# Performance work log

Measured on AMD Instinct MI355X. Metric: run time of the kernel, lower is better.

## Reference

```python
import jax, jax.numpy as jnp
import numpy as np

N = 50000     # nodes
E = 800000    # edges
D = 64        # hidesize (= out_channels per head)
H = 5         # heads
C = 64        # per-head channels (concat=False -> mean over heads, C == D)
NEG_SLOPE = 0.2
LN_EPS = 1e-5


def setup_inputs() -> dict:
    key = jax.random.key(0)
    ks = jax.random.split(key, 16)
    s = 0.05
    return {
        "features": jax.random.normal(ks[0], (N, D), dtype=jnp.float32),
        "edge_index": jax.random.randint(ks[1], (2, E), 0, N, dtype=jnp.int64),
        "rel_emb_vector": jax.random.normal(ks[2], (E, D), dtype=jnp.float32),
        # GATv2Conv params
        "Wl": jax.random.normal(ks[3], (D, H * C), dtype=jnp.float32) * s,
        "bl": jnp.zeros((H * C,), jnp.float32),
        "Wr": jax.random.normal(ks[4], (D, H * C), dtype=jnp.float32) * s,
        "br": jnp.zeros((H * C,), jnp.float32),
        "We": jax.random.normal(ks[5], (D, H * C), dtype=jnp.float32) * s,  # lin_edge, no bias
        "att": jax.random.normal(ks[6], (H, C), dtype=jnp.float32) * s,
        "conv_bias": jnp.zeros((C,), jnp.float32),
        # LayerNorms
        "ln_g": jnp.ones((D,), jnp.float32), "ln_b": jnp.zeros((D,), jnp.float32),
        "ln1_g": jnp.ones((D,), jnp.float32), "ln1_b": jnp.zeros((D,), jnp.float32),
        # MLP (activation resolved to None by the source bug)
        "fc_w": jax.random.normal(ks[7], (D, 2 * D), dtype=jnp.float32) * s,
        "fc_b": jnp.zeros((2 * D,), jnp.float32),
        "fc1_w": jax.random.normal(ks[8], (2 * D, D), dtype=jnp.float32) * s,
        "fc1_b": jnp.zeros((D,), jnp.float32),
    }


def _layernorm(x, g, b):
    m = x.mean(-1, keepdims=True)
    v = ((x - m) ** 2).mean(-1, keepdims=True)
    return (x - m) * jax.lax.rsqrt(v + LN_EPS) * g + b


def _gatv2_conv(x, edge_index, edge_attr, Wl, bl, Wr, br, We, att, conv_bias):
    src, dst = edge_index[0], edge_index[1]
    n = x.shape[0]
    # add_self_loops with fill_value='mean': self-loop edge_attr = mean of incoming edge_attr
    cnt = jax.ops.segment_sum(jnp.ones((edge_attr.shape[0],), x.dtype), dst, num_segments=n)
    loop_attr = jax.ops.segment_sum(edge_attr, dst, num_segments=n) / jnp.maximum(cnt, 1.0)[:, None]
    ar = jnp.arange(n, dtype=src.dtype)
    src2 = jnp.concatenate([src, ar])
    dst2 = jnp.concatenate([dst, ar])
    ea = jnp.concatenate([edge_attr, loop_attr], axis=0)        # [E+N, D]
    xl = (x @ Wl + bl).reshape(n, H, C)                          # source transform
    xr = (x @ Wr + br).reshape(n, H, C)                          # target transform
    em = (ea @ We).reshape(-1, H, C)
    m = jax.nn.leaky_relu(xl[src2] + xr[dst2] + em, NEG_SLOPE)   # [E+N, H, C]
    logits = jnp.einsum('ehc,hc->eh', m, att)                    # [E+N, H]
    # scatter-softmax over destination nodes (self loops guarantee nonempty segments)
    mx = jax.lax.stop_gradient(jax.ops.segment_max(logits, dst2, num_segments=n))
    z = jnp.exp(logits - mx[dst2])
    den = jax.ops.segment_sum(z, dst2, num_segments=n)
    alpha = z / den[dst2]                                        # [E+N, H]
    out = jax.ops.segment_sum(xl[src2] * alpha[:, :, None], dst2, num_segments=n)  # [N, H, C]
    return out.mean(axis=1) + conv_bias                          # concat=False -> head mean


def reference(features, edge_index, rel_emb_vector, Wl, bl, Wr, br, We, att, conv_bias,
              ln_g, ln_b, ln1_g, ln1_b, fc_w, fc_b, fc1_w, fc1_b):
    conv = _gatv2_conv(features, edge_index, rel_emb_vector, Wl, bl, Wr, br, We, att, conv_bias)
    x = _layernorm(features + conv, ln_g, ln_b)
    h = (x @ fc_w + fc_b) @ fc1_w + fc1_b   # activation=None, dropout in eval mode
    return _layernorm(x + h, ln1_g, ln1_b)
```

## Files before the change

### kernel.cpp

```cpp
#include <hip/hip_runtime.h>
#include <hip/hip_bf16.h>
#include <math.h>

#define LN_EPS 1e-5f
#define NEGS 0.2f

typedef short s8v __attribute__((ext_vector_type(8)));
typedef short s4v __attribute__((ext_vector_type(4)));
typedef float f4v __attribute__((ext_vector_type(4)));
typedef unsigned short ushort;

__device__ __forceinline__ float wredsum(float v) {
#pragma unroll
    for (int s = 32; s > 0; s >>= 1) v += __shfl_xor(v, s);
    return v;
}
__device__ __forceinline__ ushort f2bf(float x) {
    unsigned int u = __float_as_uint(x);
    u += 0x7fffu + ((u >> 16) & 1u);
    return (ushort)(u >> 16);
}
__device__ __forceinline__ float bf2f(ushort u) {
    return __uint_as_float(((unsigned int)u) << 16);
}

__global__ __launch_bounds__(256) void k_prep(const float* __restrict__ Weg,
                                              const float* __restrict__ Wlg,
                                              const float* __restrict__ Wrg,
                                              ushort* __restrict__ weTg,
                                              ushort* __restrict__ wlrTg) {
    int i = blockIdx.x * 256 + threadIdx.x;
    if (i >= 7680) return;
    int mat = i / 2560;
    int j = i - mat * 2560;
    int n = j >> 3, kb = j & 7;
    const float* W = (mat == 0) ? Weg : (mat == 1) ? Wlg : Wrg;
    s8v v;
#pragma unroll
    for (int k = 0; k < 8; k++) v[k] = (short)f2bf(W[(kb * 8 + k) * 320 + n]);
    int by = (n * 128 + kb * 16) ^ ((n & 7) << 4);
    ushort* dstp = (mat == 0) ? weTg : (wlrTg + (mat - 1) * 20480);
    *(s8v*)((char*)dstp + by) = v;
}

__global__ void k_hist(const int* __restrict__ dst, int* __restrict__ cnt, int E) {
    int idx = blockIdx.x * blockDim.x + threadIdx.x;
    int stride = gridDim.x * blockDim.x;
    for (; idx < E; idx += stride) atomicAdd(&cnt[dst[idx]], 1);
}

__global__ __launch_bounds__(1024) void k_scanA(const int* __restrict__ cnt,
                                                int* __restrict__ bsum, int N) {
    __shared__ int ws[16];
    int tt = threadIdx.x, ln = tt & 63, wv = tt >> 6;
    int i = blockIdx.x * 1024 + tt;
    int v = (i < N) ? (cnt[i] + 1) : 0;
#pragma unroll
    for (int s = 32; s > 0; s >>= 1) v += __shfl_xor(v, s);
    if (ln == 0) ws[wv] = v;
    __syncthreads();
    if (tt == 0) {
        int s = 0;
#pragma unroll
        for (int k = 0; k < 16; k++) s += ws[k];
        bsum[blockIdx.x] = s;
    }
}
__global__ __launch_bounds__(64) void k_scanB(const int* __restrict__ bsum,
                                              int* __restrict__ bpre,
                                              int* __restrict__ roffN, int nb) {
    int ln = threadIdx.x;
    int v = (ln < nb) ? bsum[ln] : 0;
    int x = v;
#pragma unroll
    for (int off = 1; off < 64; off <<= 1) {
        int y = __shfl_up(x, off);
        if (ln >= off) x += y;
    }
    if (ln < nb) bpre[ln] = x - v;
    if (ln == 63) *roffN = x;
}
__global__ __launch_bounds__(1024) void k_scanC(const int* __restrict__ cnt,
                                                const int* __restrict__ bpre,
                                                int* __restrict__ roff,
                                                int* __restrict__ wpos, int N) {
    __shared__ int ws[16];
    int tt = threadIdx.x, ln = tt & 63, wv = tt >> 6;
    int i = blockIdx.x * 1024 + tt;
    int v = (i < N) ? (cnt[i] + 1) : 0;
    int x = v;
#pragma unroll
    for (int off = 1; off < 64; off <<= 1) {
        int y = __shfl_up(x, off);
        if (ln >= off) x += y;
    }
    if (ln == 63) ws[wv] = x;
    __syncthreads();
    if (wv == 0) {
        int wsv = (ln < 16) ? ws[ln] : 0;
        int xs = wsv;
#pragma unroll
        for (int off = 1; off < 16; off <<= 1) {
            int y = __shfl_up(xs, off);
            if (ln >= off) xs += y;
        }
        if (ln < 16) ws[ln] = xs - wsv;
    }
    __syncthreads();
    int excl = x - v + ws[wv] + bpre[blockIdx.x];
    if (i < N) { roff[i] = excl; wpos[i] = excl; }
}

__global__ void k_scatter(const int* __restrict__ src, const int* __restrict__ dst,
                          int* __restrict__ wpos, int* __restrict__ eidC,
                          int* __restrict__ srcC, int* __restrict__ dstC, int E) {
    int idx = blockIdx.x * blockDim.x + threadIdx.x;
    int stride = gridDim.x * blockDim.x;
    for (; idx < E; idx += stride) {
        int d = dst[idx];
        int p = atomicAdd(&wpos[d], 1);
        eidC[p] = idx;
        srcC[p] = src[idx];
        dstC[p] = d;
    }
}

__global__ __launch_bounds__(256) void k_loopcsr(const int* __restrict__ eidC_ro,
                                                 const int* __restrict__ roff,
                                                 const float* __restrict__ rel,
                                                 float* __restrict__ loopat,
                                                 int* __restrict__ eidC,
                                                 int* __restrict__ srcC,
                                                 int* __restrict__ dstC, int N, int E) {
    int t = threadIdx.x, ln = t & 63, wv = t >> 6;
    int nw = gridDim.x * 4;
    for (int n = blockIdx.x * 4 + wv; n < N; n += nw) {
        int r0 = roff[n], r1 = roff[n + 1];
        int deg = r1 - r0 - 1;
        float s0 = 0.f, s1 = 0.f, s2 = 0.f, s3 = 0.f;
        int j = 0;
        for (; j + 4 <= deg; j += 4) {
            int e0 = eidC_ro[r0 + j], e1 = eidC_ro[r0 + j + 1];
            int e2 = eidC_ro[r0 + j + 2], e3 = eidC_ro[r0 + j + 3];
            s0 += rel[(long long)e0 * 64 + ln];
            s1 += rel[(long long)e1 * 64 + ln];
            s2 += rel[(long long)e2 * 64 + ln];
            s3 += rel[(long long)e3 * 64 + ln];
        }
        for (; j < deg; j++) s0 += rel[(long long)eidC_ro[r0 + j] * 64 + ln];
        float s = (s0 + s1) + (s2 + s3);
        loopat[(long long)n * 64 + ln] = s / (float)(deg > 0 ? deg : 1);
        if (ln == 0) {
            eidC[r1 - 1] = E + n;
            srcC[r1 - 1] = n;
            dstC[r1 - 1] = n;
        }
    }
}

__global__ __launch_bounds__(512) void k_linC(const float* __restrict__ feat,
                                              const ushort* __restrict__ wlrTg,
                                              const float* __restrict__ blg,
                                              const float* __restrict__ brg,
                                              ushort* __restrict__ xlbf,
                                              ushort* __restrict__ xrbf, int N) {
    __shared__ __align__(16) ushort wT[2][64 * 320];
    int t = threadIdx.x;
    {
        const s8v* wsrc = (const s8v*)wlrTg;
        s8v* wdst = (s8v*)&wT[0][0];
        for (int i = t; i < 5120; i += 512) wdst[i] = wsrc[i];
    }
    __syncthreads();

    int l = t & 63, wv = t >> 6;
    int g = l >> 4, m = l & 15;
    int wstride = gridDim.x * 128;
    for (int r0 = (blockIdx.x * 8 + wv) * 16; r0 < N; r0 += wstride) {
        s8v afr[2];
        {
            long long row = (r0 + m < N) ? (r0 + m) : (N - 1);
#pragma unroll
            for (int kh = 0; kh < 2; kh++) {
                const float* p = feat + row * 64 + kh * 32 + g * 8;
                float4 u0 = *(const float4*)(p);
                float4 u1 = *(const float4*)(p + 4);
                s8v a;
                a[0] = (short)f2bf(u0.x); a[1] = (short)f2bf(u0.y);
                a[2] = (short)f2bf(u0.z); a[3] = (short)f2bf(u0.w);
                a[4] = (short)f2bf(u1.x); a[5] = (short)f2bf(u1.y);
                a[6] = (short)f2bf(u1.z); a[7] = (short)f2bf(u1.w);
                afr[kh] = a;
            }
        }
#pragma unroll
        for (int mat = 0; mat < 2; mat++) {
            const float* bias = mat ? brg : blg;
            ushort* y = mat ? xrbf : xlbf;
            const char* wb = (const char*)&wT[mat][0];
#pragma unroll
            for (int h = 0; h < 5; h++) {
                f4v acc[4];
#pragma unroll
                for (int ct = 0; ct < 4; ct++) acc[ct] = (f4v)0.0f;
#pragma unroll
                for (int ct = 0; ct < 4; ct++) {
                    int n = h * 64 + ct * 16 + m;
                    int b0 = (n * 128 + 0 * 64 + g * 16) ^ ((n & 7) << 4);
                    int b1 = (n * 128 + 1 * 64 + g * 16) ^ ((n & 7) << 4);
                    s8v bf0 = *(const s8v*)(wb + b0);
                    s8v bf1 = *(const s8v*)(wb + b1);
                    acc[ct] = __builtin_amdgcn_mfma_f32_16x16x32_bf16(afr[0], bf0, acc[ct], 0, 0, 0);
                    acc[ct] = __builtin_amdgcn_mfma_f32_16x16x32_bf16(afr[1], bf1, acc[ct], 0, 0, 0);
                }
                float bv[4];
#pragma unroll
                for (int ct = 0; ct < 4; ct++) bv[ct] = bias[h * 64 + ct * 16 + m];
#pragma unroll
                for (int q = 0; q < 4; q++) {
                    int row = r0 + g * 4 + q;
                    if (row < N) {
                        s4v o;
#pragma unroll
                        for (int ct = 0; ct < 4; ct++) o[ct] = (short)f2bf(acc[ct][q] + bv[ct]);
                        *(s4v*)(y + (long long)row * 320 + h * 64 + m * 4) = o;
                    }
                }
            }
        }
    }
}

__global__ __launch_bounds__(512) void k_fused(
    const float* __restrict__ rel, const float* __restrict__ loopat,
    const int* __restrict__ eidC, const int* __restrict__ srcC,
    const int* __restrict__ dstC,
    const ushort* __restrict__ xlbf, const ushort* __restrict__ xrbf,
    const ushort* __restrict__ weTg, const float* __restrict__ attg,
    float* __restrict__ logitsC, int E, int M) {
    __shared__ __align__(16) ushort weT[64 * 320];
    int t = threadIdx.x;
    {
        const s8v* wsrc = (const s8v*)weTg;
        s8v* wdst = (s8v*)weT;
        for (int i = t; i < 2560; i += 512) wdst[i] = wsrc[i];
    }
    __syncthreads();

    int l = t & 63, wv = t >> 6;
    int g = l >> 4, m = l & 15;
    int r0 = (blockIdx.x * 8 + wv) * 16;
    if (r0 >= M) return;

    s8v afr[2];
    {
        int slot = r0 + m;
        if (slot >= M) slot = M - 1;
        int e = eidC[slot];
        const float* ap = (e < E) ? (rel + (long long)e * 64)
                                  : (loopat + (long long)(e - E) * 64);
#pragma unroll
        for (int kh = 0; kh < 2; kh++) {
            const float* p = ap + kh * 32 + g * 8;
            float4 u0 = *(const float4*)(p);
            float4 u1 = *(const float4*)(p + 4);
            s8v a;
            a[0] = (short)f2bf(u0.x); a[1] = (short)f2bf(u0.y);
            a[2] = (short)f2bf(u0.z); a[3] = (short)f2bf(u0.w);
            a[4] = (short)f2bf(u1.x); a[5] = (short)f2bf(u1.y);
            a[6] = (short)f2bf(u1.z); a[7] = (short)f2bf(u1.w);
            afr[kh] = a;
        }
    }

    const ushort* xptr[4];
    const ushort* rptr[4];
    bool vld[4];
    int sarr[4];
#pragma unroll
    for (int q = 0; q < 4; q++) {
        int slot = r0 + g * 4 + q;
        vld[q] = slot < M;
        int ss = vld[q] ? slot : (M - 1);
        sarr[q] = ss;
        int s = srcC[ss], d = dstC[ss];
        xptr[q] = xlbf + (long long)s * 320 + m * 4;
        rptr[q] = xrbf + (long long)d * 320 + m * 4;
    }

    s4v xb[2][4], rb[2][4];
    float attb[2][4];
#pragma unroll
    for (int q = 0; q < 4; q++) {
        xb[0][q] = *(const s4v*)(xptr[q]);
        rb[0][q] = *(const s4v*)(rptr[q]);
    }
#pragma unroll
    for (int ct = 0; ct < 4; ct++) attb[0][ct] = attg[ct * 16 + m];

#pragma unroll
    for (int h = 0; h < 5; h++) {
        if (h < 4) {
#pragma unroll
            for (int q = 0; q < 4; q++) {
                xb[(h + 1) & 1][q] = *(const s4v*)(xptr[q] + (h + 1) * 64);
                rb[(h + 1) & 1][q] = *(const s4v*)(rptr[q] + (h + 1) * 64);
            }
#pragma unroll
            for (int ct = 0; ct < 4; ct++)
                attb[(h + 1) & 1][ct] = attg[(h + 1) * 64 + ct * 16 + m];
        }

        f4v acc[4];
#pragma unroll
        for (int ct = 0; ct < 4; ct++) acc[ct] = (f4v)0.0f;
#pragma unroll
        for (int ct = 0; ct < 4; ct++) {
            int n = h * 64 + ct * 16 + m;
            int b0 = (n * 128 + 0 * 64 + g * 16) ^ ((n & 7) << 4);
            int b1 = (n * 128 + 1 * 64 + g * 16) ^ ((n & 7) << 4);
            s8v bf0 = *(const s8v*)((const char*)weT + b0);
            s8v bf1 = *(const s8v*)((const char*)weT + b1);
            acc[ct] = __builtin_amdgcn_mfma_f32_16x16x32_bf16(afr[0], bf0, acc[ct], 0, 0, 0);
            acc[ct] = __builtin_amdgcn_mfma_f32_16x16x32_bf16(afr[1], bf1, acc[ct], 0, 0, 0);
        }

#pragma unroll
        for (int q = 0; q < 4; q++) {
            float sum = 0.f;
#pragma unroll
            for (int ct = 0; ct < 4; ct++) {
                float v = acc[ct][q] + bf2f((ushort)xb[h & 1][q][ct])
                                     + bf2f((ushort)rb[h & 1][q][ct]);
                v = v > 0.f ? v : v * NEGS;
                sum = fmaf(v, attb[h & 1][ct], sum);
            }
            sum += __shfl_xor(sum, 1);
            sum += __shfl_xor(sum, 2);
            sum += __shfl_xor(sum, 4);
            sum += __shfl_xor(sum, 8);
            if (vld[q] && m == 0) logitsC[(long long)sarr[q] * 5 + h] = sum;
        }
    }
}

__global__ __launch_bounds__(256) void k_agg(const float* __restrict__ logitsC,
                                             const int* __restrict__ srcC,
                                             const int* __restrict__ roff,
                                             const ushort* __restrict__ xlbf,
                                             float* __restrict__ conv, int N) {
    int t = threadIdx.x, ln = t & 63, wv = t >> 6;
    int sub = ln >> 4, m = ln & 15;
    int nw = gridDim.x * 4;
    for (int n = blockIdx.x * 4 + wv; n < N; n += nw) {
        int r0 = roff[n], r1 = roff[n + 1];
        int deg = r1 - r0;
        float se[5] = {0.f, 0.f, 0.f, 0.f, 0.f};
        for (int j = ln; j < deg; j += 64) {
            long long base = (long long)(r0 + j) * 5;
#pragma unroll
            for (int h = 0; h < 5; h++) se[h] += expf(logitsC[base + h]);
        }
        float dh[5];
#pragma unroll
        for (int h = 0; h < 5; h++) dh[h] = 1.0f / wredsum(se[h]);
        float accv[4] = {0.f, 0.f, 0.f, 0.f};
        for (int jj = sub; jj < deg; jj += 4) {
            int slot = r0 + jj;
            int s = srcC[slot];
            const ushort* xp = xlbf + (long long)s * 320 + m * 4;
            long long lb = (long long)slot * 5;
#pragma unroll
            for (int h = 0; h < 5; h++) {
                float a = expf(logitsC[lb + h]) * dh[h];
                s4v xv = *(const s4v*)(xp + h * 64);
#pragma unroll
                for (int j = 0; j < 4; j++) accv[j] = fmaf(a, bf2f((ushort)xv[j]), accv[j]);
            }
        }
#pragma unroll
        for (int j = 0; j < 4; j++) {
            accv[j] += __shfl_xor(accv[j], 16);
            accv[j] += __shfl_xor(accv[j], 32);
        }
        float v0 = __shfl(accv[0], m);
        float v1 = __shfl(accv[1], m);
        float v2 = __shfl(accv[2], m);
        float v3 = __shfl(accv[3], m);
        float outv = (sub == 0) ? v0 : (sub == 1) ? v1 : (sub == 2) ? v2 : v3;
        conv[(long long)n * 64 + ln] = outv * 0.2f;
    }
}

__global__ __launch_bounds__(512) void k_mlp(const float* __restrict__ feat,
                                             const float* __restrict__ conv,
                                             const float* __restrict__ cbias,
                                             const float* __restrict__ lng,
                                             const float* __restrict__ lnb,
                                             const float* __restrict__ ln1g,
                                             const float* __restrict__ ln1b,
                                             const float* __restrict__ fcwg,
                                             const float* __restrict__ fcb,
                                             const float* __restrict__ fc1wg,
                                             const float* __restrict__ fc1b,
                                             float* __restrict__ out, int N) {
    __shared__ __align__(16) ushort w1T[64 * 128];
    __shared__ __align__(16) ushort w2T[64 * 128];
    __shared__ __align__(16) ushort tls[8][16 * 128];
    __shared__ __align__(16) ushort xnl[8][16 * 64];
    int t = threadIdx.x;
    for (int i = t; i < 8192; i += 512) {
        int k = i >> 7, n = i & 127;
        int by = (n * 128 + k * 2) ^ ((n & 7) << 4);
        w1T[by >> 1] = f2bf(fcwg[i]);
    }
    for (int i = t; i < 8192; i += 512) {
        int k = i >> 6, n = i & 63;
        int by = (n * 256 + k * 2) ^ ((n & 7) << 4);
        w2T[by >> 1] = f2bf(fc1wg[i]);
    }
    __syncthreads();
    int ln = t & 63, wv = t >> 6;
    int g = ln >> 4, m = ln & 15;
    char* tb = (char*)&tls[wv][0];
    char* xb = (char*)&xnl[wv][0];
    float fcbv[8];
#pragma unroll
    for (int ct = 0; ct < 8; ct++) fcbv[ct] = fcb[ct * 16 + m];
    float fc1bv[4], g1v[4], b1v[4];
#pragma unroll
    for (int ct = 0; ct < 4; ct++) {
        fc1bv[ct] = fc1b[ct * 16 + m];
        g1v[ct] = ln1g[ct * 16 + m];
        b1v[ct] = ln1b[ct * 16 + m];
    }
    int nblk = gridDim.x * 8;
    for (int nb0 = (blockIdx.x * 8 + wv) * 16; nb0 < N; nb0 += nblk * 16) {
        int node = nb0 + m;
        long long nd = (node < N) ? node : (N - 1);
        float xv[2][8];
#pragma unroll
        for (int kh = 0; kh < 2; kh++) {
            int c0 = kh * 32 + g * 8;
            const float* fp = feat + nd * 64 + c0;
            const float* cp = conv + nd * 64 + c0;
            float4 f0 = *(const float4*)fp, f1 = *(const float4*)(fp + 4);
            float4 q0 = *(const float4*)cp, q1 = *(const float4*)(cp + 4);
            float4 cb0 = *(const float4*)(cbias + c0), cb1 = *(const float4*)(cbias + c0 + 4);
            xv[kh][0] = f0.x + q0.x + cb0.x; xv[kh][1] = f0.y + q0.y + cb0.y;
            xv[kh][2] = f0.z + q0.z + cb0.z; xv[kh][3] = f0.w + q0.w + cb0.w;
            xv[kh][4] = f1.x + q1.x + cb1.x; xv[kh][5] = f1.y + q1.y + cb1.y;
            xv[kh][6] = f1.z + q1.z + cb1.z; xv[kh][7] = f1.w + q1.w + cb1.w;
        }
        float sm = 0.f;
#pragma unroll
        for (int kh = 0; kh < 2; kh++)
#pragma unroll
            for (int j = 0; j < 8; j++) sm += xv[kh][j];
        sm += __shfl_xor(sm, 16); sm += __shfl_xor(sm, 32);
        float mu = sm * (1.0f / 64.0f);
        float vr = 0.f;
#pragma unroll
        for (int kh = 0; kh < 2; kh++)
#pragma unroll
            for (int j = 0; j < 8; j++) {
                float dv = xv[kh][j] - mu;
                vr += dv * dv;
            }
        vr += __shfl_xor(vr, 16); vr += __shfl_xor(vr, 32);
        float rs = rsqrtf(vr * (1.0f / 64.0f) + LN_EPS);
        s8v af[2];
#pragma unroll
        for (int kh = 0; kh < 2; kh++) {
            int c0 = kh * 32 + g * 8;
            float4 g0 = *(const float4*)(lng + c0), g1 = *(const float4*)(lng + c0 + 4);
            float4 e0 = *(const float4*)(lnb + c0), e1 = *(const float4*)(lnb + c0 + 4);
            float gg[8] = {g0.x, g0.y, g0.z, g0.w, g1.x, g1.y, g1.z, g1.w};
            float bb[8] = {e0.x, e0.y, e0.z, e0.w, e1.x, e1.y, e1.z, e1.w};
#pragma unroll
            for (int j = 0; j < 8; j++)
                af[kh][j] = (short)f2bf((xv[kh][j] - mu) * rs * gg[j] + bb[j]);
            int by = (m * 128 + (kh * 32 + g * 8) * 2) ^ ((m & 7) << 4);
            *(s8v*)(xb + by) = af[kh];
        }
        f4v a1[8];
#pragma unroll
        for (int ct = 0; ct < 8; ct++) a1[ct] = (f4v)0.0f;
#pragma unroll
        for (int ct = 0; ct < 8; ct++) {
            int n1 = ct * 16 + m;
#pragma unroll
            for (int kh = 0; kh < 2; kh++) {
                int by = (n1 * 128 + (kh * 32 + g * 8) * 2) ^ ((n1 & 7) << 4);
                s8v bf = *(const s8v*)((const char*)w1T + by);
                a1[ct] = __builtin_amdgcn_mfma_f32_16x16x32_bf16(af[kh], bf, a1[ct], 0, 0, 0);
            }
        }
#pragma unroll
        for (int ct = 0; ct < 8; ct++)
#pragma unroll
            for (int q = 0; q < 4; q++) {
                int r = g * 4 + q, c = ct * 16 + m;
                int by = (r * 256 + c * 2) ^ ((r & 7) << 4);
                *(ushort*)(tb + by) = f2bf(a1[ct][q] + fcbv[ct]);
            }
        f4v a2[4];
#pragma unroll
        for (int ct = 0; ct < 4; ct++) a2[ct] = (f4v)0.0f;
#pragma unroll
        for (int kh2 = 0; kh2 < 4; kh2++) {
            int by = (m * 256 + (kh2 * 32 + g * 8) * 2) ^ ((m & 7) << 4);
            s8v a2f = *(const s8v*)(tb + by);
#pragma unroll
            for (int ct = 0; ct < 4; ct++) {
                int n2 = ct * 16 + m;
                int by2 = (n2 * 256 + (kh2 * 32 + g * 8) * 2) ^ ((n2 & 7) << 4);
                s8v bf = *(const s8v*)((const char*)w2T + by2);
                a2[ct] = __builtin_amdgcn_mfma_f32_16x16x32_bf16(a2f, bf, a2[ct], 0, 0, 0);
            }
        }
#pragma unroll
        for (int q = 0; q < 4; q++) {
            int r = g * 4 + q;
            float yv[4];
#pragma unroll
            for (int ct = 0; ct < 4; ct++) {
                int by = (r * 128 + (ct * 16 + m) * 2) ^ ((r & 7) << 4);
                yv[ct] = bf2f(*(const ushort*)(xb + by)) + a2[ct][q] + fc1bv[ct];
            }
            float sm2 = (yv[0] + yv[1]) + (yv[2] + yv[3]);
            sm2 += __shfl_xor(sm2, 1); sm2 += __shfl_xor(sm2, 2);
            sm2 += __shfl_xor(sm2, 4); sm2 += __shfl_xor(sm2, 8);
            float mu2 = sm2 * (1.0f / 64.0f);
            float vr2 = 0.f;
#pragma unroll
            for (int ct = 0; ct < 4; ct++) {
                float dv = yv[ct] - mu2;
                vr2 += dv * dv;
            }
            vr2 += __shfl_xor(vr2, 1); vr2 += __shfl_xor(vr2, 2);
            vr2 += __shfl_xor(vr2, 4); vr2 += __shfl_xor(vr2, 8);
            float rs2 = rsqrtf(vr2 * (1.0f / 64.0f) + LN_EPS);
            int rn = nb0 + r;
            if (rn < N) {
#pragma unroll
                for (int ct = 0; ct < 4; ct++)
                    out[(long long)rn * 64 + ct * 16 + m] =
                        (yv[ct] - mu2) * rs2 * g1v[ct] + b1v[ct];
            }
        }
    }
}

extern "C" void kernel_launch(void* const* d_in, const int* in_sizes, int n_in,
                              void* d_out, int out_size, void* d_ws, size_t ws_size,
                              hipStream_t stream) {
    const float* feat = (const float*)d_in[0];
    const int* ei = (const int*)d_in[1];
    const float* rel = (const float*)d_in[2];
    const float* Wl = (const float*)d_in[3];
    const float* bl = (const float*)d_in[4];
    const float* Wr = (const float*)d_in[5];
    const float* br = (const float*)d_in[6];
    const float* We = (const float*)d_in[7];
    const float* att = (const float*)d_in[8];
    const float* cbias = (const float*)d_in[9];
    const float* lng = (const float*)d_in[10];
    const float* lnb = (const float*)d_in[11];
    const float* ln1g = (const float*)d_in[12];
    const float* ln1b = (const float*)d_in[13];
    const float* fcw = (const float*)d_in[14];
    const float* fcb = (const float*)d_in[15];
    const float* fc1w = (const float*)d_in[16];
    const float* fc1b = (const float*)d_in[17];
    float* out = (float*)d_out;

    int N = in_sizes[0] / 64;
    int E = in_sizes[1] / 2;
    int M = E + N;
    const int* src = ei;
    const int* dst = ei + E;
    int nb = (N + 1023) / 1024;

    char* wsb = (char*)d_ws;
    ushort* xlbf = (ushort*)wsb;            wsb += (size_t)N * 320 * 2;
    ushort* xrbf = (ushort*)wsb;            wsb += (size_t)N * 320 * 2;
    float* loopat = (float*)wsb;            wsb += (size_t)N * 64 * 4;
    float* conv = (float*)wsb;              wsb += (size_t)N * 64 * 4;
    ushort* weTg = (ushort*)wsb;            wsb += 40960;
    ushort* wlrTg = (ushort*)wsb;           wsb += 81920;
    float* logitsC = (float*)wsb;           wsb += (size_t)M * 5 * 4;
    int* cnt = (int*)wsb;                   wsb += (size_t)N * 4;
    int* roff = (int*)wsb;                  wsb += (size_t)(N + 1) * 4;
    int* wpos = (int*)wsb;                  wsb += (size_t)N * 4;
    int* eidC = (int*)wsb;                  wsb += (size_t)M * 4;
    int* srcC = (int*)wsb;                  wsb += (size_t)M * 4;
    int* dstC = (int*)wsb;                  wsb += (size_t)M * 4;
    int* bsum = (int*)wsb;                  wsb += 64 * 4;
    int* bpre = (int*)wsb;                  wsb += 64 * 4;

    hipMemsetAsync(cnt, 0, (size_t)N * 4, stream);

    k_prep<<<30, 256, 0, stream>>>(We, Wl, Wr, weTg, wlrTg);
    k_hist<<<1024, 256, 0, stream>>>(dst, cnt, E);
    k_scanA<<<nb, 1024, 0, stream>>>(cnt, bsum, N);
    k_scanB<<<1, 64, 0, stream>>>(bsum, bpre, &roff[N], nb);
    k_scanC<<<nb, 1024, 0, stream>>>(cnt, bpre, roff, wpos, N);
    k_scatter<<<1024, 256, 0, stream>>>(src, dst, wpos, eidC, srcC, dstC, E);
    k_loopcsr<<<2048, 256, 0, stream>>>(eidC, roff, rel, loopat, eidC, srcC, dstC, N, E);
    k_linC<<<(N + 127) / 128, 512, 0, stream>>>(feat, wlrTg, bl, br, xlbf, xrbf, N);
    k_fused<<<(M + 127) / 128, 512, 0, stream>>>(rel, loopat, eidC, srcC, dstC,
                                                 xlbf, xrbf, weTg, att, logitsC, E, M);
    k_agg<<<2048, 256, 0, stream>>>(logitsC, srcC, roff, xlbf, conv, N);
    k_mlp<<<391, 512, 0, stream>>>(feat, conv, cbias, lng, lnb, ln1g, ln1b, fcw, fcb, fc1w, fc1b,
                                   out, N);
}
```

Measured before the change: 514.0 us.

## Pre-permute edge features to bf16 CSR order and fuse softmax denominators via atomics

```diff
diff --git a/kernel.cpp b/kernel.cpp
--- a/kernel.cpp
+++ b/kernel.cpp
@@ -129,6 +129,7 @@
                                                  const int* __restrict__ roff,
                                                  const float* __restrict__ rel,
                                                  float* __restrict__ loopat,
+                                                 ushort* __restrict__ relbf,
                                                  int* __restrict__ eidC,
                                                  int* __restrict__ srcC,
                                                  int* __restrict__ dstC, int N, int E) {
@@ -138,18 +139,43 @@
         int r0 = roff[n], r1 = roff[n + 1];
         int deg = r1 - r0 - 1;
         float s0 = 0.f, s1 = 0.f, s2 = 0.f, s3 = 0.f;
-        int j = 0;
-        for (; j + 4 <= deg; j += 4) {
-            int e0 = eidC_ro[r0 + j], e1 = eidC_ro[r0 + j + 1];
-            int e2 = eidC_ro[r0 + j + 2], e3 = eidC_ro[r0 + j + 3];
-            s0 += rel[(long long)e0 * 64 + ln];
-            s1 += rel[(long long)e1 * 64 + ln];
-            s2 += rel[(long long)e2 * 64 + ln];
-            s3 += rel[(long long)e3 * 64 + ln];
-        }
-        for (; j < deg; j++) s0 += rel[(long long)eidC_ro[r0 + j] * 64 + ln];
-        float s = (s0 + s1) + (s2 + s3);
-        loopat[(long long)n * 64 + ln] = s / (float)(deg > 0 ? deg : 1);
+        if (relbf) {
+            int j = 0;
+            for (; j + 4 <= deg; j += 4) {
+                int e0 = eidC_ro[r0 + j], e1 = eidC_ro[r0 + j + 1];
+                int e2 = eidC_ro[r0 + j + 2], e3 = eidC_ro[r0 + j + 3];
+                float v0 = rel[(long long)e0 * 64 + ln];
+                float v1 = rel[(long long)e1 * 64 + ln];
+                float v2 = rel[(long long)e2 * 64 + ln];
+                float v3 = rel[(long long)e3 * 64 + ln];
+                s0 += v0; s1 += v1; s2 += v2; s3 += v3;
+                relbf[(long long)(r0 + j) * 64 + ln] = f2bf(v0);
+                relbf[(long long)(r0 + j + 1) * 64 + ln] = f2bf(v1);
+                relbf[(long long)(r0 + j + 2) * 64 + ln] = f2bf(v2);
+                relbf[(long long)(r0 + j + 3) * 64 + ln] = f2bf(v3);
+            }
+            for (; j < deg; j++) {
+                float v = rel[(long long)eidC_ro[r0 + j] * 64 + ln];
+                s0 += v;
+                relbf[(long long)(r0 + j) * 64 + ln] = f2bf(v);
+            }
+            float s = (s0 + s1) + (s2 + s3);
+            float mean = s / (float)(deg > 0 ? deg : 1);
+            relbf[(long long)(r1 - 1) * 64 + ln] = f2bf(mean);
+        } else {
+            int j = 0;
+            for (; j + 4 <= deg; j += 4) {
+                int e0 = eidC_ro[r0 + j], e1 = eidC_ro[r0 + j + 1];
+                int e2 = eidC_ro[r0 + j + 2], e3 = eidC_ro[r0 + j + 3];
+                s0 += rel[(long long)e0 * 64 + ln];
+                s1 += rel[(long long)e1 * 64 + ln];
+                s2 += rel[(long long)e2 * 64 + ln];
+                s3 += rel[(long long)e3 * 64 + ln];
+            }
+            for (; j < deg; j++) s0 += rel[(long long)eidC_ro[r0 + j] * 64 + ln];
+            float s = (s0 + s1) + (s2 + s3);
+            loopat[(long long)n * 64 + ln] = s / (float)(deg > 0 ? deg : 1);
+        }
         if (ln == 0) {
             eidC[r1 - 1] = E + n;
             srcC[r1 - 1] = n;
@@ -231,13 +257,15 @@
     }
 }
 
+template <bool RELBF>
 __global__ __launch_bounds__(512) void k_fused(
     const float* __restrict__ rel, const float* __restrict__ loopat,
+    const ushort* __restrict__ relbf,
     const int* __restrict__ eidC, const int* __restrict__ srcC,
     const int* __restrict__ dstC,
     const ushort* __restrict__ xlbf, const ushort* __restrict__ xrbf,
     const ushort* __restrict__ weTg, const float* __restrict__ attg,
-    float* __restrict__ logitsC, int E, int M) {
+    float* __restrict__ zC, float* __restrict__ den, int E, int M) {
     __shared__ __align__(16) ushort weT[64 * 320];
     int t = threadIdx.x;
     {
@@ -253,7 +281,13 @@
     if (r0 >= M) return;
 
     s8v afr[2];
-    {
+    if constexpr (RELBF) {
+        int slot = r0 + m;
+        if (slot >= M) slot = M - 1;
+        const ushort* p = relbf + (long long)slot * 64 + g * 8;
+        afr[0] = *(const s8v*)(p);
+        afr[1] = *(const s8v*)(p + 32);
+    } else {
         int slot = r0 + m;
         if (slot >= M) slot = M - 1;
         int e = eidC[slot];
@@ -276,7 +310,7 @@
     const ushort* xptr[4];
     const ushort* rptr[4];
     bool vld[4];
-    int sarr[4];
+    int sarr[4], darr[4];
 #pragma unroll
     for (int q = 0; q < 4; q++) {
         int slot = r0 + g * 4 + q;
@@ -284,6 +318,7 @@
         int ss = vld[q] ? slot : (M - 1);
         sarr[q] = ss;
         int s = srcC[ss], d = dstC[ss];
+        darr[q] = d;
         xptr[q] = xlbf + (long long)s * 320 + m * 4;
         rptr[q] = xrbf + (long long)d * 320 + m * 4;
     }
@@ -339,12 +374,17 @@
             sum += __shfl_xor(sum, 2);
             sum += __shfl_xor(sum, 4);
             sum += __shfl_xor(sum, 8);
-            if (vld[q] && m == 0) logitsC[(long long)sarr[q] * 5 + h] = sum;
-        }
-    }
-}
-
-__global__ __launch_bounds__(256) void k_agg(const float* __restrict__ logitsC,
+            if (vld[q] && m == 0) {
+                float z = __expf(sum);
+                zC[(long long)sarr[q] * 5 + h] = z;
+                atomicAdd(&den[(long long)darr[q] * 5 + h], z);
+            }
+        }
+    }
+}
+
+__global__ __launch_bounds__(256) void k_agg(const float* __restrict__ zC,
+                                             const float* __restrict__ den,
                                              const int* __restrict__ srcC,
                                              const int* __restrict__ roff,
                                              const ushort* __restrict__ xlbf,
@@ -355,15 +395,9 @@
     for (int n = blockIdx.x * 4 + wv; n < N; n += nw) {
         int r0 = roff[n], r1 = roff[n + 1];
         int deg = r1 - r0;
-        float se[5] = {0.f, 0.f, 0.f, 0.f, 0.f};
-        for (int j = ln; j < deg; j += 64) {
-            long long base = (long long)(r0 + j) * 5;
-#pragma unroll
-            for (int h = 0; h < 5; h++) se[h] += expf(logitsC[base + h]);
-        }
         float dh[5];
 #pragma unroll
-        for (int h = 0; h < 5; h++) dh[h] = 1.0f / wredsum(se[h]);
+        for (int h = 0; h < 5; h++) dh[h] = 1.0f / den[(long long)n * 5 + h];
         float accv[4] = {0.f, 0.f, 0.f, 0.f};
         for (int jj = sub; jj < deg; jj += 4) {
             int slot = r0 + jj;
@@ -372,7 +406,7 @@
             long long lb = (long long)slot * 5;
 #pragma unroll
             for (int h = 0; h < 5; h++) {
-                float a = expf(logitsC[lb + h]) * dh[h];
+                float a = zC[lb + h] * dh[h];
                 s4v xv = *(const s4v*)(xp + h * 64);
 #pragma unroll
                 for (int j = 0; j < 4; j++) accv[j] = fmaf(a, bf2f((ushort)xv[j]), accv[j]);
@@ -589,7 +623,8 @@
     float* conv = (float*)wsb;              wsb += (size_t)N * 64 * 4;
     ushort* weTg = (ushort*)wsb;            wsb += 40960;
     ushort* wlrTg = (ushort*)wsb;           wsb += 81920;
-    float* logitsC = (float*)wsb;           wsb += (size_t)M * 5 * 4;
+    float* zC = (float*)wsb;                wsb += (size_t)M * 5 * 4;
+    float* den = (float*)wsb;               wsb += (size_t)N * 5 * 4;
     int* cnt = (int*)wsb;                   wsb += (size_t)N * 4;
     int* roff = (int*)wsb;                  wsb += (size_t)(N + 1) * 4;
     int* wpos = (int*)wsb;                  wsb += (size_t)N * 4;
@@ -599,7 +634,13 @@
     int* bsum = (int*)wsb;                  wsb += 64 * 4;
     int* bpre = (int*)wsb;                  wsb += 64 * 4;
 
+    size_t used = (size_t)(wsb - (char*)d_ws);
+    size_t roff_relbf = (used + 15) & ~(size_t)15;
+    bool use_relbf = (roff_relbf + (size_t)M * 128) <= ws_size;
+    ushort* relbf = use_relbf ? (ushort*)((char*)d_ws + roff_relbf) : nullptr;
+
     hipMemsetAsync(cnt, 0, (size_t)N * 4, stream);
+    hipMemsetAsync(den, 0, (size_t)N * 5 * 4, stream);
 
     k_prep<<<30, 256, 0, stream>>>(We, Wl, Wr, weTg, wlrTg);
     k_hist<<<1024, 256, 0, stream>>>(dst, cnt, E);
@@ -607,11 +648,15 @@
     k_scanB<<<1, 64, 0, stream>>>(bsum, bpre, &roff[N], nb);
     k_scanC<<<nb, 1024, 0, stream>>>(cnt, bpre, roff, wpos, N);
     k_scatter<<<1024, 256, 0, stream>>>(src, dst, wpos, eidC, srcC, dstC, E);
-    k_loopcsr<<<2048, 256, 0, stream>>>(eidC, roff, rel, loopat, eidC, srcC, dstC, N, E);
+    k_loopcsr<<<2048, 256, 0, stream>>>(eidC, roff, rel, loopat, relbf, eidC, srcC, dstC, N, E);
     k_linC<<<(N + 127) / 128, 512, 0, stream>>>(feat, wlrTg, bl, br, xlbf, xrbf, N);
-    k_fused<<<(M + 127) / 128, 512, 0, stream>>>(rel, loopat, eidC, srcC, dstC,
-                                                 xlbf, xrbf, weTg, att, logitsC, E, M);
-    k_agg<<<2048, 256, 0, stream>>>(logitsC, srcC, roff, xlbf, conv, N);
+    if (use_relbf)
+        k_fused<true><<<(M + 127) / 128, 512, 0, stream>>>(rel, loopat, relbf, eidC, srcC, dstC,
+                                                           xlbf, xrbf, weTg, att, zC, den, E, M);
+    else
+        k_fused<false><<<(M + 127) / 128, 512, 0, stream>>>(rel, loopat, relbf, eidC, srcC, dstC,
+                                                            xlbf, xrbf, weTg, att, zC, den, E, M);
+    k_agg<<<2048, 256, 0, stream>>>(zC, den, srcC, roff, xlbf, conv, N);
     k_mlp<<<391, 512, 0, stream>>>(feat, conv, cbias, lng, lnb, ln1g, ln1b, fcw, fcb, fc1w, fc1b,
                                    out, N);
 }
```

Measured after the change: 608.2 us. 1.18x slower.
